# Performance work log

Measured on AMD Instinct MI355X. Metric: run time of the kernel, lower is better.

## Reference

```python
import jax, jax.numpy as jnp
import numpy as np

CUT = 512          # cut_size
H = W = 4096       # sideY, sideX (square -> reflect pad in original is a no-op)
N_INNER = 12       # cut_innercut[999-300]
CUT_POW = 1.0
GRAY_W = (0.2989, 0.587, 0.114)  # torchvision rgb_to_grayscale weights


def _gray(x):
    # x: [..., 3, h, w] -> replicate luma over 3 channels (T.Grayscale(3))
    w = jnp.asarray(GRAY_W, x.dtype)
    g = jnp.einsum('...chw,c->...hw', x, w)
    return jnp.broadcast_to(g[..., None, :, :], x.shape)


def _crop_resize(img, offy, offx, size):
    # Bilinear resize of img[:, offy:offy+size, offx:offx+size] to [3, CUT, CUT].
    # Implements crop+resize as a fused bilinear gather (align_corners=False mapping).
    s = size.astype(jnp.float32)
    t = (jnp.arange(CUT, dtype=jnp.float32) + 0.5) * s / CUT - 0.5
    y = jnp.clip(offy + t, offy, offy + s - 1.0)
    x = jnp.clip(offx + t, offx, offx + s - 1.0)
    y0 = jnp.floor(y).astype(jnp.int32)
    x0 = jnp.floor(x).astype(jnp.int32)
    y1 = jnp.minimum(y0 + 1, offy + size - 1)
    x1 = jnp.minimum(x0 + 1, offx + size - 1)
    wy = (y - y0)[None, :, None]
    wx = (x - x0)[None, None, :]
    g = lambda yy, xx: img[:, yy][:, :, xx]  # [3, CUT, CUT]
    top = g(y0, x0) * (1.0 - wx) + g(y0, x1) * wx
    bot = g(y1, x0) * (1.0 - wx) + g(y1, x1) * wx
    return top * (1.0 - wy) + bot * wy


def setup_inputs() -> dict:
    key = jax.random.key(0)
    k1, k2, k3, k4 = jax.random.split(key, 4)
    inp = jax.random.uniform(k1, (1, 3, H, W), jnp.float32)
    min_size = min(H, W, CUT)
    max_size = min(H, W)
    u = jax.random.uniform(k2, (N_INNER,))
    sizes = (u ** CUT_POW * (max_size - min_size) + min_size).astype(jnp.int32)
    offy = (jax.random.uniform(k3, (N_INNER,)) * (H - sizes + 1)).astype(jnp.int32)
    offx = (jax.random.uniform(k4, (N_INNER,)) * (W - sizes + 1)).astype(jnp.int32)
    return {"input": inp, "t": 300, "sizes": sizes, "offy": offy, "offx": offx}


def reference(input, t, sizes, offy, offx):
    # t=300 -> overview=4, inner_crop=12, ic_grey_p=0 (counts baked into static shapes)
    img = input[0]  # [3, H, W]; reflect pad is a no-op for a square image
    full = _crop_resize(img, jnp.int32(0), jnp.int32(0), jnp.int32(min(H, W)))
    flipped = full[..., ::-1]
    overview = jnp.stack([full, _gray(full), flipped, _gray(flipped)])  # [4,3,CUT,CUT]
    inner = jax.vmap(lambda oy, ox, s: _crop_resize(img, oy, ox, s))(offy, offx, sizes)
    # i <= int(0 * 12) -> only inner crop 0 is grayscaled
    inner = inner.at[0].set(_gray(inner[0]))
    return jnp.concatenate([overview, inner], axis=0)  # [16, 3, CUT, CUT]
```

## Files before the change

kernel.cpp:

```cpp
#include <hip/hip_runtime.h>

#define CUT 512
#define HH 4096
#define WW 4096
#define SPAN 2048
#define NIMG 13

__device__ __forceinline__ int sw(int x) { return x ^ ((x >> 5) & 31); }

__device__ __forceinline__ void coord(int i, int off, int size, float s,
                                      int& c0, int& c1, float& w) {
    float t = ((i + 0.5f) * s) / 512.0f - 0.5f;
    float offf = (float)off;
    float v = off + t;
    v = fminf(fmaxf(v, offf), offf + s - 1.0f);
    c0 = (int)floorf(v);
    c1 = min(c0 + 1, off + size - 1);
    w = v - (float)c0;
}

__global__ __launch_bounds__(256)
void cutouts_kernel(const float* __restrict__ img,
                    const int* __restrict__ sizes,
                    const int* __restrict__ offy,
                    const int* __restrict__ offx,
                    float* __restrict__ out) {
    __shared__ float rows[3][2][SPAN];

    const int z   = blockIdx.z;
    const int i   = blockIdx.y;
    const int jt  = blockIdx.x * 256;
    const int tid = threadIdx.x;
    const int j   = jt + tid;

    int size, oy, ox;
    if (z == 0) { size = 4096; oy = 0; ox = 0; }
    else        { size = sizes[z - 1]; oy = offy[z - 1]; ox = offx[z - 1]; }
    const float s = (float)size;

    int y0, y1; float wy;
    coord(i, oy, size, s, y0, y1, wy);

    int xlo, xhi, dmy; float wd;
    coord(jt,       ox, size, s, xlo, dmy, wd);
    coord(jt + 255, ox, size, s, dmy, xhi, wd);
    const int span = xhi - xlo + 1;

    const float* r00 = img + (size_t)0 * HH * WW + (size_t)y0 * WW + xlo;
    const float* r01 = img + (size_t)0 * HH * WW + (size_t)y1 * WW + xlo;
    const float* r10 = img + (size_t)1 * HH * WW + (size_t)y0 * WW + xlo;
    const float* r11 = img + (size_t)1 * HH * WW + (size_t)y1 * WW + xlo;
    const float* r20 = img + (size_t)2 * HH * WW + (size_t)y0 * WW + xlo;
    const float* r21 = img + (size_t)2 * HH * WW + (size_t)y1 * WW + xlo;

    for (int idx = tid; idx < span; idx += 256) {
        int si = sw(idx);
        rows[0][0][si] = r00[idx];
        rows[0][1][si] = r01[idx];
        rows[1][0][si] = r10[idx];
        rows[1][1][si] = r11[idx];
        rows[2][0][si] = r20[idx];
        rows[2][1][si] = r21[idx];
    }
    __syncthreads();

    int x0, x1; float wx;
    coord(j, ox, size, s, x0, x1, wx);
    const int l0 = sw(x0 - xlo);
    const int l1 = sw(x1 - xlo);

    float v[3];
#pragma unroll
    for (int c = 0; c < 3; ++c) {
        float a = rows[c][0][l0];
        float b = rows[c][0][l1];
        float cc = rows[c][1][l0];
        float d = rows[c][1][l1];
        float top = a * (1.0f - wx) + b * wx;
        float bot = cc * (1.0f - wx) + d * wx;
        v[c] = top * (1.0f - wy) + bot * wy;
    }

    const size_t imgStride = (size_t)3 * CUT * CUT;
    const size_t chStride  = (size_t)CUT * CUT;
    const size_t px  = (size_t)i * CUT + j;

    if (z == 0) {
        float gray = v[0] * 0.2989f + v[1] * 0.587f + v[2] * 0.114f;
        const size_t pxf = (size_t)i * CUT + (CUT - 1 - j);
#pragma unroll
        for (int c = 0; c < 3; ++c) {
            out[0 * imgStride + c * chStride + px]  = v[c];
            out[1 * imgStride + c * chStride + px]  = gray;
            out[2 * imgStride + c * chStride + pxf] = v[c];
            out[3 * imgStride + c * chStride + pxf] = gray;
        }
    } else {
        const int k = z - 1;
        const size_t base = (size_t)(4 + k) * imgStride;
        if (k == 0) {
            float gray = v[0] * 0.2989f + v[1] * 0.587f + v[2] * 0.114f;
#pragma unroll
            for (int c = 0; c < 3; ++c)
                out[base + c * chStride + px] = gray;
        } else {
#pragma unroll
            for (int c = 0; c < 3; ++c)
                out[base + c * chStride + px] = v[c];
        }
    }
}

extern "C" void kernel_launch(void* const* d_in, const int* in_sizes, int n_in,
                              void* d_out, int out_size, void* d_ws, size_t ws_size,
                              hipStream_t stream) {
    const float* img  = (const float*)d_in[0];
    const int* sizes  = (const int*)d_in[2];
    const int* offy   = (const int*)d_in[3];
    const int* offx   = (const int*)d_in[4];
    float* out = (float*)d_out;

    dim3 block(256, 1, 1);
    dim3 grid(CUT / 256, CUT, NIMG);
    hipLaunchKernelGGL(cutouts_kernel, grid, block, 0, stream,
                       img, sizes, offy, offx, out);
}
```

Measured before the change: 312.2 us.

## Split bilinear crop-resize into separable horizontal and vertical passes

Replaces the single kernel, which staged full contiguous source-row spans into LDS, with two kernels. The first gathers only the two needed source pixels per output column for each (image, row, tap, channel) and writes horizontal interpolations to a workspace buffer. The second reads those values back, applies the vertical blend and writes the overview, flipped, grey and inner outputs. This avoids loading unused pixels into LDS and drops the block-level sync. The cost is a large intermediate buffer written and read through global memory, plus a second launch.

Result: slower. 330.9 us (+6.0%).

```diff
diff --git a/kernel.cpp b/kernel.cpp
--- a/kernel.cpp
+++ b/kernel.cpp
@@ -3,10 +3,6 @@
 #define CUT 512
 #define HH 4096
 #define WW 4096
-#define SPAN 2048
-#define NIMG 13
-
-__device__ __forceinline__ int sw(int x) { return x ^ ((x >> 5) & 31); }
 
 __device__ __forceinline__ void coord(int i, int off, int size, float s,
                                       int& c0, int& c1, float& w) {
@@ -19,71 +15,77 @@
     w = v - (float)c0;
 }
 
+__device__ __forceinline__ void getParams(int imgI,
+                                          const int* __restrict__ sizes,
+                                          const int* __restrict__ offy,
+                                          const int* __restrict__ offx,
+                                          int& size, int& oy, int& ox) {
+    if (imgI == 0) { size = 4096; oy = 0; ox = 0; }
+    else { size = sizes[imgI - 1]; oy = offy[imgI - 1]; ox = offx[imgI - 1]; }
+}
+
 __global__ __launch_bounds__(256)
-void cutouts_kernel(const float* __restrict__ img,
-                    const int* __restrict__ sizes,
-                    const int* __restrict__ offy,
-                    const int* __restrict__ offx,
-                    float* __restrict__ out) {
-    __shared__ float rows[3][2][SPAN];
-
-    const int z   = blockIdx.z;
-    const int i   = blockIdx.y;
-    const int jt  = blockIdx.x * 256;
-    const int tid = threadIdx.x;
-    const int j   = jt + tid;
+void pass1_kernel(const float* __restrict__ img,
+                  const int* __restrict__ sizes,
+                  const int* __restrict__ offy,
+                  const int* __restrict__ offx,
+                  float* __restrict__ tmp) {
+    const int zz   = blockIdx.z;
+    const int imgI = zz / 6;
+    const int rc   = zz % 6;
+    const int r    = rc / 3;
+    const int c    = rc % 3;
+    const int i    = blockIdx.y;
+    const int j    = blockIdx.x * 256 + threadIdx.x;
 
     int size, oy, ox;
-    if (z == 0) { size = 4096; oy = 0; ox = 0; }
-    else        { size = sizes[z - 1]; oy = offy[z - 1]; ox = offx[z - 1]; }
+    getParams(imgI, sizes, offy, offx, size, oy, ox);
+    const float s = (float)size;
+
+    int y0, y1; float wy;
+    coord(i, oy, size, s, y0, y1, wy);
+    const int yr = r ? y1 : y0;
+
+    int x0, x1; float wx;
+    coord(j, ox, size, s, x0, x1, wx);
+
+    const float* p = img + (size_t)c * HH * WW + (size_t)yr * WW;
+    float a = p[x0];
+    float b = p[x1];
+    float h = a * (1.0f - wx) + b * wx;
+
+    tmp[((((size_t)imgI * CUT + i) * 2 + r) * 3 + c) * CUT + j] = h;
+}
+
+__global__ __launch_bounds__(256)
+void pass2_kernel(const int* __restrict__ sizes,
+                  const int* __restrict__ offy,
+                  const int* __restrict__ offx,
+                  const float* __restrict__ tmp,
+                  float* __restrict__ out) {
+    const int z = blockIdx.z;
+    const int i = blockIdx.y;
+    const int j = blockIdx.x * 256 + threadIdx.x;
+
+    int size, oy, ox;
+    getParams(z, sizes, offy, offx, size, oy, ox);
     const float s = (float)size;
 
     int y0, y1; float wy;
     coord(i, oy, size, s, y0, y1, wy);
 
-    int xlo, xhi, dmy; float wd;
-    coord(jt,       ox, size, s, xlo, dmy, wd);
-    coord(jt + 255, ox, size, s, dmy, xhi, wd);
-    const int span = xhi - xlo + 1;
-
-    const float* r00 = img + (size_t)0 * HH * WW + (size_t)y0 * WW + xlo;
-    const float* r01 = img + (size_t)0 * HH * WW + (size_t)y1 * WW + xlo;
-    const float* r10 = img + (size_t)1 * HH * WW + (size_t)y0 * WW + xlo;
-    const float* r11 = img + (size_t)1 * HH * WW + (size_t)y1 * WW + xlo;
-    const float* r20 = img + (size_t)2 * HH * WW + (size_t)y0 * WW + xlo;
-    const float* r21 = img + (size_t)2 * HH * WW + (size_t)y1 * WW + xlo;
-
-    for (int idx = tid; idx < span; idx += 256) {
-        int si = sw(idx);
-        rows[0][0][si] = r00[idx];
-        rows[0][1][si] = r01[idx];
-        rows[1][0][si] = r10[idx];
-        rows[1][1][si] = r11[idx];
-        rows[2][0][si] = r20[idx];
-        rows[2][1][si] = r21[idx];
-    }
-    __syncthreads();
-
-    int x0, x1; float wx;
-    coord(j, ox, size, s, x0, x1, wx);
-    const int l0 = sw(x0 - xlo);
-    const int l1 = sw(x1 - xlo);
-
+    const size_t tbase = (((size_t)z * CUT + i) * 2) * 3 * CUT;
     float v[3];
 #pragma unroll
     for (int c = 0; c < 3; ++c) {
-        float a = rows[c][0][l0];
-        float b = rows[c][0][l1];
-        float cc = rows[c][1][l0];
-        float d = rows[c][1][l1];
-        float top = a * (1.0f - wx) + b * wx;
-        float bot = cc * (1.0f - wx) + d * wx;
+        float top = tmp[tbase + (size_t)c * CUT + j];
+        float bot = tmp[tbase + (size_t)(3 + c) * CUT + j];
         v[c] = top * (1.0f - wy) + bot * wy;
     }
 
     const size_t imgStride = (size_t)3 * CUT * CUT;
     const size_t chStride  = (size_t)CUT * CUT;
-    const size_t px  = (size_t)i * CUT + j;
+    const size_t px = (size_t)i * CUT + j;
 
     if (z == 0) {
         float gray = v[0] * 0.2989f + v[1] * 0.587f + v[2] * 0.114f;
@@ -119,9 +121,14 @@
     const int* offy   = (const int*)d_in[3];
     const int* offx   = (const int*)d_in[4];
     float* out = (float*)d_out;
+    float* tmp = (float*)d_ws;
 
     dim3 block(256, 1, 1);
-    dim3 grid(CUT / 256, CUT, NIMG);
-    hipLaunchKernelGGL(cutouts_kernel, grid, block, 0, stream,
-                       img, sizes, offy, offx, out);
+    dim3 grid1(CUT / 256, CUT, 13 * 6);
+    hipLaunchKernelGGL(pass1_kernel, grid1, block, 0, stream,
+                       img, sizes, offy, offx, tmp);
+
+    dim3 grid2(CUT / 256, CUT, 13);
+    hipLaunchKernelGGL(pass2_kernel, grid2, block, 0, stream,
+                       sizes, offy, offx, tmp, out);
 }
```

## Replace LDS row staging with direct paired global gathers and nontemporal stores

Applied to the files above, without the earlier changes.

Drops the shared-memory staging of whole source row spans, along with its barrier. Each thread now loads its two horizontal neighbours straight from global memory as one 8-byte vector load per row and channel, with edge handling done by shifting the base index. This avoids loading full spans of up to 2048 floats per row when only 512 samples are needed, which matters for large crops. Output writes become nontemporal stores to reduce cache pollution. The trade-off is less coalesced gathers and reliance on cache hits when adjacent threads share source pixels.

Result: faster. 293.3 us (-6.1%).

```diff
diff --git a/kernel.cpp b/kernel.cpp
--- a/kernel.cpp
+++ b/kernel.cpp
@@ -3,10 +3,8 @@
 #define CUT 512
 #define HH 4096
 #define WW 4096
-#define SPAN 2048
-#define NIMG 13
 
-__device__ __forceinline__ int sw(int x) { return x ^ ((x >> 5) & 31); }
+typedef float v2f __attribute__((ext_vector_type(2), aligned(4)));
 
 __device__ __forceinline__ void coord(int i, int off, int size, float s,
                                       int& c0, int& c1, float& w) {
@@ -25,13 +23,9 @@
                     const int* __restrict__ offy,
                     const int* __restrict__ offx,
                     float* __restrict__ out) {
-    __shared__ float rows[3][2][SPAN];
-
-    const int z   = blockIdx.z;
-    const int i   = blockIdx.y;
-    const int jt  = blockIdx.x * 256;
-    const int tid = threadIdx.x;
-    const int j   = jt + tid;
+    const int z = blockIdx.z;
+    const int i = blockIdx.y;
+    const int j = blockIdx.x * 256 + threadIdx.x;
 
     int size, oy, ox;
     if (z == 0) { size = 4096; oy = 0; ox = 0; }
@@ -40,60 +34,42 @@
 
     int y0, y1; float wy;
     coord(i, oy, size, s, y0, y1, wy);
-
-    int xlo, xhi, dmy; float wd;
-    coord(jt,       ox, size, s, xlo, dmy, wd);
-    coord(jt + 255, ox, size, s, dmy, xhi, wd);
-    const int span = xhi - xlo + 1;
-
-    const float* r00 = img + (size_t)0 * HH * WW + (size_t)y0 * WW + xlo;
-    const float* r01 = img + (size_t)0 * HH * WW + (size_t)y1 * WW + xlo;
-    const float* r10 = img + (size_t)1 * HH * WW + (size_t)y0 * WW + xlo;
-    const float* r11 = img + (size_t)1 * HH * WW + (size_t)y1 * WW + xlo;
-    const float* r20 = img + (size_t)2 * HH * WW + (size_t)y0 * WW + xlo;
-    const float* r21 = img + (size_t)2 * HH * WW + (size_t)y1 * WW + xlo;
-
-    for (int idx = tid; idx < span; idx += 256) {
-        int si = sw(idx);
-        rows[0][0][si] = r00[idx];
-        rows[0][1][si] = r01[idx];
-        rows[1][0][si] = r10[idx];
-        rows[1][1][si] = r11[idx];
-        rows[2][0][si] = r20[idx];
-        rows[2][1][si] = r21[idx];
-    }
-    __syncthreads();
-
     int x0, x1; float wx;
     coord(j, ox, size, s, x0, x1, wx);
-    const int l0 = sw(x0 - xlo);
-    const int l1 = sw(x1 - xlo);
+
+    const bool xe = (x0 >= ox + size - 1);
+    const int  xb = xe ? x0 - 1 : x0;
 
     float v[3];
 #pragma unroll
     for (int c = 0; c < 3; ++c) {
-        float a = rows[c][0][l0];
-        float b = rows[c][0][l1];
-        float cc = rows[c][1][l0];
-        float d = rows[c][1][l1];
-        float top = a * (1.0f - wx) + b * wx;
+        const float* base = img + (size_t)c * HH * WW;
+        const float* r0 = base + (size_t)y0 * WW + xb;
+        const float* r1 = base + (size_t)y1 * WW + xb;
+        v2f t2 = *(const v2f*)r0;
+        v2f b2 = *(const v2f*)r1;
+        float a  = xe ? t2.y : t2.x;
+        float b  = t2.y;
+        float cc = xe ? b2.y : b2.x;
+        float d  = b2.y;
+        float top = a  * (1.0f - wx) + b * wx;
         float bot = cc * (1.0f - wx) + d * wx;
         v[c] = top * (1.0f - wy) + bot * wy;
     }
 
     const size_t imgStride = (size_t)3 * CUT * CUT;
     const size_t chStride  = (size_t)CUT * CUT;
-    const size_t px  = (size_t)i * CUT + j;
+    const size_t px = (size_t)i * CUT + j;
 
     if (z == 0) {
         float gray = v[0] * 0.2989f + v[1] * 0.587f + v[2] * 0.114f;
         const size_t pxf = (size_t)i * CUT + (CUT - 1 - j);
 #pragma unroll
         for (int c = 0; c < 3; ++c) {
-            out[0 * imgStride + c * chStride + px]  = v[c];
-            out[1 * imgStride + c * chStride + px]  = gray;
-            out[2 * imgStride + c * chStride + pxf] = v[c];
-            out[3 * imgStride + c * chStride + pxf] = gray;
+            __builtin_nontemporal_store(v[c],  &out[0 * imgStride + c * chStride + px]);
+            __builtin_nontemporal_store(gray,  &out[1 * imgStride + c * chStride + px]);
+            __builtin_nontemporal_store(v[c],  &out[2 * imgStride + c * chStride + pxf]);
+            __builtin_nontemporal_store(gray,  &out[3 * imgStride + c * chStride + pxf]);
         }
     } else {
         const int k = z - 1;
@@ -102,11 +78,11 @@
             float gray = v[0] * 0.2989f + v[1] * 0.587f + v[2] * 0.114f;
 #pragma unroll
             for (int c = 0; c < 3; ++c)
-                out[base + c * chStride + px] = gray;
+                __builtin_nontemporal_store(gray, &out[base + c * chStride + px]);
         } else {
 #pragma unroll
             for (int c = 0; c < 3; ++c)
-                out[base + c * chStride + px] = v[c];
+                __builtin_nontemporal_store(v[c], &out[base + c * chStride + px]);
         }
     }
 }
@@ -121,7 +97,7 @@
     float* out = (float*)d_out;
 
     dim3 block(256, 1, 1);
-    dim3 grid(CUT / 256, CUT, NIMG);
+    dim3 grid(CUT / 256, CUT, 13);
     hipLaunchKernelGGL(cutouts_kernel, grid, block, 0, stream,
                        img, sizes, offy, offx, out);
 }
```
